# Optimization experiments

Measured on AMD Instinct MI355X. Metric: run time of the kernel, lower is better.

The kernel has to match this reference:

```python
import jax, jax.numpy as jnp
import numpy as np

N_NODES = 50000
N_EDGES = 800000
IN_DIM = 256
HID = 256
NUM_LAYERS = 2


def _sage(xin, src, dst, inv_deg, W_l, b_l, W_r):
    # PyG SAGEConv (mean aggr): lin_l(mean of src features scattered to dst) + lin_r(x)
    agg = jax.ops.segment_sum(xin[src], dst, num_segments=xin.shape[0]) * inv_deg
    return agg @ W_l + b_l + xin @ W_r


def _mgdsgu(x, src, dst, inv_deg, h, Wx_l, bx_l, Wx_r, Wh_l, bh_l, Wh_r, Wb1, bb1, Wb2, bb2):
    # hid->hid conv order: 0=sage_hidden, 1=sage_single_h, 2=sage_update_h, 3=sage_candidate_h
    # in ->hid conv order: 0=sage_single_x, 1=sage_update_x, 2=sage_candidate_x
    h_N = _sage(h, src, dst, inv_deg, Wh_l[0], bh_l[0], Wh_r[0])
    # predict_missing_info: r = zeros so r_v = beta; gamma is computed in the
    # original but multiplied by zero -> no effect (omitted).
    beta = jnp.tanh(h @ Wb1 + bb1 + h_N @ Wb2 + bb2)
    m = h + beta - h_N
    h_N = h_N + m  # == h + beta, kept as written for clarity
    r = jax.nn.sigmoid(_sage(x, src, dst, inv_deg, Wx_l[0], bx_l[0], Wx_r[0])
                       + _sage(h_N, src, dst, inv_deg, Wh_l[1], bh_l[1], Wh_r[1]))
    z = jax.nn.sigmoid(_sage(x, src, dst, inv_deg, Wx_l[1], bx_l[1], Wx_r[1])
                       + _sage(h_N, src, dst, inv_deg, Wh_l[2], bh_l[2], Wh_r[2]))
    h_tilde = jnp.tanh(_sage(x, src, dst, inv_deg, Wx_l[2], bx_l[2], Wx_r[2])
                       + _sage(r * h_N, src, dst, inv_deg, Wh_l[3], bh_l[3], Wh_r[3]))
    return (1.0 - z) * h_N + z * h_tilde


def setup_inputs() -> dict:
    key = jax.random.key(0)
    ks = jax.random.split(key, 12)
    sx = 1.0 / np.sqrt(IN_DIM)
    sh = 1.0 / np.sqrt(HID)
    inp = {
        "x": jax.random.normal(ks[0], (N_NODES, IN_DIM), dtype=jnp.float32),
        "edge_index": jax.random.randint(ks[1], (2, N_EDGES), 0, N_NODES, dtype=jnp.int64),
        "Wx_l": jax.random.normal(ks[2], (3, IN_DIM, HID), dtype=jnp.float32) * sx,
        "bx_l": jnp.zeros((3, HID), dtype=jnp.float32),
        "Wx_r": jax.random.normal(ks[3], (3, IN_DIM, HID), dtype=jnp.float32) * sx,
        "Wh_l": jax.random.normal(ks[4], (4, HID, HID), dtype=jnp.float32) * sh,
        "bh_l": jnp.zeros((4, HID), dtype=jnp.float32),
        "Wh_r": jax.random.normal(ks[5], (4, HID, HID), dtype=jnp.float32) * sh,
        "Wb1": jax.random.normal(ks[6], (HID, HID), dtype=jnp.float32) * sh,
        "bb1": jnp.zeros((HID,), dtype=jnp.float32),
        "Wb2": jax.random.normal(ks[7], (HID, HID), dtype=jnp.float32) * sh,
        "bb2": jnp.zeros((HID,), dtype=jnp.float32),
        "We1": jax.random.normal(ks[8], (2 * HID, HID), dtype=jnp.float32) * (1.0 / np.sqrt(2 * HID)),
        "be1": jnp.zeros((HID,), dtype=jnp.float32),
        "We2": jax.random.normal(ks[9], (HID, 1), dtype=jnp.float32) * sh,
        "be2": jnp.zeros((1,), dtype=jnp.float32),
    }
    return inp


def reference(x, edge_index, Wx_l, bx_l, Wx_r, Wh_l, bh_l, Wh_r,
              Wb1, bb1, Wb2, bb2, We1, be1, We2, be2):
    src, dst = edge_index[0], edge_index[1]
    deg = jax.ops.segment_sum(jnp.ones((src.shape[0],), dtype=x.dtype), dst,
                              num_segments=x.shape[0])
    inv_deg = (1.0 / jnp.maximum(deg, 1.0))[:, None]  # [N, 1]

    h = jnp.zeros((x.shape[0], HID), dtype=x.dtype)
    for _ in range(NUM_LAYERS):
        h = _mgdsgu(x, src, dst, inv_deg, h, Wx_l, bx_l, Wx_r,
                    Wh_l, bh_l, Wh_r, Wb1, bb1, Wb2, bb2)

    # edge embeddings: concat(src emb, dst emb) -> MLP -> sigmoid
    edge_emb = jnp.concatenate([h[src], h[dst]], axis=1)  # [E, 2H]
    hidden = jax.nn.relu(edge_emb @ We1 + be1)
    preds = jax.nn.sigmoid(hidden @ We2 + be2)  # [E, 1]
    return (preds, h)
```

## Files before the change

### kernel.cpp

```cpp
#include <hip/hip_runtime.h>
#include <math.h>

#define HID 256

typedef __bf16 bf16x8 __attribute__((ext_vector_type(8)));
typedef float  f32x4  __attribute__((ext_vector_type(4)));

__device__ __forceinline__ float sigmoidf_(float x){ return 1.0f/(1.0f + __expf(-x)); }
__device__ __forceinline__ unsigned short f2b(float f){
  __bf16 b = (__bf16)f; return __builtin_bit_cast(unsigned short, b);
}
__device__ __forceinline__ float b2f(unsigned short u){
  return (float)__builtin_bit_cast(__bf16, u);
}

__device__ __forceinline__ int edge_src(const int* ei, int e, int is64){
  return is64 ? ei[2*e] : ei[e];
}
__device__ __forceinline__ int edge_dst(const int* ei, int e, int E, int is64){
  return is64 ? ei[2*(E+e)] : ei[E+e];
}

__global__ void detect_kernel(const int* __restrict__ ei, int* __restrict__ flag){
  __shared__ int any;
  if (threadIdx.x == 0) any = 0;
  __syncthreads();
  if (ei[2*threadIdx.x + 1] != 0) atomicOr(&any, 1);
  __syncthreads();
  if (threadIdx.x == 0) *flag = any ? 0 : 1;
}

__global__ void count_kernel(const int* __restrict__ ei, const int* __restrict__ flag,
                             int* __restrict__ deg_i, int E){
  int e = blockIdx.x*blockDim.x + threadIdx.x;
  if (e >= E) return;
  int is64 = *flag;
  atomicAdd(&deg_i[edge_dst(ei,e,E,is64)], 1);
}

__global__ __launch_bounds__(1024) void scan_kernel(const int* __restrict__ deg_i,
  int* __restrict__ row_ptr, float* __restrict__ inv_deg, int N)
{
  __shared__ int wsum[16];
  __shared__ int carry_s;
  int tid = threadIdx.x, lane = tid & 63, wid = tid >> 6;
  if (tid == 0) carry_s = 0;
  __syncthreads();
  for (int base = 0; base < N; base += 1024){
    int i = base + tid;
    int v = (i < N) ? deg_i[i] : 0;
    int s = v;
    #pragma unroll
    for (int off = 1; off < 64; off <<= 1){
      int t = __shfl_up(s, off, 64);
      if (lane >= off) s += t;
    }
    if (lane == 63) wsum[wid] = s;
    __syncthreads();
    if (tid == 0){
      int run = 0;
      for (int w2 = 0; w2 < 16; ++w2){ int t = wsum[w2]; wsum[w2] = run; run += t; }
    }
    __syncthreads();
    int excl = carry_s + wsum[wid] + s - v;
    if (i < N){
      row_ptr[i] = excl;
      inv_deg[i] = 1.0f / fmaxf((float)v, 1.0f);
    }
    __syncthreads();
    if (tid == 1023) carry_s = excl + v;
    __syncthreads();
  }
  if (threadIdx.x == 0) row_ptr[N] = carry_s;
}

__global__ void fill_kernel(const int* __restrict__ ei, const int* __restrict__ flag,
                            const int* __restrict__ row_ptr, int* __restrict__ cursor,
                            int* __restrict__ col_src, int E){
  int e = blockIdx.x*blockDim.x + threadIdx.x;
  if (e >= E) return;
  int is64 = *flag;
  int d = edge_dst(ei,e,E,is64);
  int pos = atomicAdd(&cursor[d], 1);
  col_src[row_ptr[d] + pos] = edge_src(ei,e,is64);
}

__global__ __launch_bounds__(256) void conv_kernel(const float* __restrict__ in,
                                                   unsigned short* __restrict__ out, int n4){
  int i = blockIdx.x*256 + threadIdx.x;
  if (i >= n4) return;
  float4 v = *(const float4*)&in[(size_t)i*4];
  ushort4 o; o.x=f2b(v.x); o.y=f2b(v.y); o.z=f2b(v.z); o.w=f2b(v.w);
  *(ushort4*)&out[(size_t)i*4] = o;
}

__global__ __launch_bounds__(256) void wconv_kernel(
  const float* __restrict__ Wx_l, const float* __restrict__ Wx_r,
  const float* __restrict__ Wh_l, const float* __restrict__ Wh_r,
  const float* __restrict__ Wb1,  const float* __restrict__ Wb2,
  const float* __restrict__ We1,  unsigned short* __restrict__ Wt)
{
  int widx = blockIdx.x;
  int n = blockIdx.y;
  int k = threadIdx.x;
  const float* src;
  if      (widx < 3)  src = Wx_l + widx*65536;
  else if (widx < 6)  src = Wx_r + (widx-3)*65536;
  else if (widx < 10) src = Wh_l + (widx-6)*65536;
  else if (widx < 14) src = Wh_r + (widx-10)*65536;
  else if (widx == 14) src = Wb1;
  else if (widx == 15) src = Wb2;
  else                src = We1 + (widx-16)*65536;
  Wt[(size_t)widx*65536 + n*256 + k] = f2b(src[k*256 + n]);
}

__global__ __launch_bounds__(256) void aggregate_b_kernel(
    const unsigned short* __restrict__ X, unsigned short* __restrict__ out,
    const int* __restrict__ row_ptr, const int* __restrict__ col_src,
    const float* __restrict__ inv_deg, int N)
{
  int v = blockIdx.x*4 + (threadIdx.x >> 6);
  int lane = threadIdx.x & 63;
  if (v >= N) return;
  int beg = row_ptr[v], end = row_ptr[v+1];
  float a0=0.f, a1=0.f, a2=0.f, a3=0.f;
  int e = beg;
  for (; e + 4 <= end; e += 4){
    int s0 = col_src[e], s1 = col_src[e+1], s2 = col_src[e+2], s3 = col_src[e+3];
    ushort4 u0 = *(const ushort4*)&X[(size_t)s0*HID + lane*4];
    ushort4 u1 = *(const ushort4*)&X[(size_t)s1*HID + lane*4];
    ushort4 u2 = *(const ushort4*)&X[(size_t)s2*HID + lane*4];
    ushort4 u3 = *(const ushort4*)&X[(size_t)s3*HID + lane*4];
    a0 += b2f(u0.x)+b2f(u1.x)+b2f(u2.x)+b2f(u3.x);
    a1 += b2f(u0.y)+b2f(u1.y)+b2f(u2.y)+b2f(u3.y);
    a2 += b2f(u0.z)+b2f(u1.z)+b2f(u2.z)+b2f(u3.z);
    a3 += b2f(u0.w)+b2f(u1.w)+b2f(u2.w)+b2f(u3.w);
  }
  for (; e < end; ++e){
    int s0 = col_src[e];
    ushort4 u0 = *(const ushort4*)&X[(size_t)s0*HID + lane*4];
    a0 += b2f(u0.x); a1 += b2f(u0.y); a2 += b2f(u0.z); a3 += b2f(u0.w);
  }
  float w = inv_deg[v];
  ushort4 o; o.x=f2b(a0*w); o.y=f2b(a1*w); o.z=f2b(a2*w); o.w=f2b(a3*w);
  *(ushort4*)&out[(size_t)v*HID + lane*4] = o;
}

__global__ __launch_bounds__(256) void rowprep_kernel(
  const float* __restrict__ bh_l, const float* __restrict__ bb1, const float* __restrict__ bb2,
  const float* __restrict__ Wb2, const float* __restrict__ Wh_l, const float* __restrict__ Wh_r,
  float* __restrict__ hrow, float* __restrict__ rowL1, float* __restrict__ rowR1,
  float* __restrict__ rowL2, float* __restrict__ rowR2)
{
  __shared__ float sh[256];
  __shared__ float sh2[256];
  int j = threadIdx.x;
  sh[j] = bh_l[j];
  __syncthreads();
  float acc = bb1[j] + bb2[j];
  for (int k = 0; k < 256; ++k) acc = fmaf(sh[k], Wb2[k*256 + j], acc);
  float hr = tanhf(acc);
  hrow[j] = hr; sh2[j] = hr;
  __syncthreads();
  const float* Whl1 = Wh_l + 65536;  const float* Whr1 = Wh_r + 65536;
  const float* Whl2 = Wh_l + 131072; const float* Whr2 = Wh_r + 131072;
  float a1=0.f, b1=0.f, a2=0.f, b2v=0.f;
  for (int k = 0; k < 256; ++k){
    float hv = sh2[k];
    a1  = fmaf(hv, Whl1[k*256+j], a1);
    b1  = fmaf(hv, Whr1[k*256+j], b1);
    a2  = fmaf(hv, Whl2[k*256+j], a2);
    b2v = fmaf(hv, Whr2[k*256+j], b2v);
  }
  rowL1[j] = a1; rowR1[j] = b1 + bh_l[256 + j];
  rowL2[j] = a2; rowR2[j] = b2v + bh_l[512 + j];
}

template<int MODE>
__global__ __launch_bounds__(256) void mgemm_kernel(
    const unsigned short* __restrict__ A0, const unsigned short* __restrict__ W0,
    const unsigned short* __restrict__ A1, const unsigned short* __restrict__ W1,
    const unsigned short* __restrict__ A2, const unsigned short* __restrict__ W2,
    const unsigned short* __restrict__ A3, const unsigned short* __restrict__ W3,
    const float* __restrict__ bias, const float* __restrict__ bias2,
    const float* Z, const float* HN, int hn_bcast,
    const float* __restrict__ rowA, const float* __restrict__ rowB,
    const float* __restrict__ mulrow, const float* mulmat,
    const int* __restrict__ deg,
    float* outF, unsigned short* outB, int M)
{
  __shared__ unsigned short Al[128*32];
  __shared__ unsigned short Bl[128*32];
  const int tid  = threadIdx.x;
  const int lane = tid & 63, w = tid >> 6;
  const int wr = w >> 1, wc = w & 1;
  const int lane15 = lane & 15, laneq = (lane >> 4) * 8;
  const int row0 = blockIdx.x * 128, col0 = blockIdx.y * 128;

  f32x4 acc[4][4];
  #pragma unroll
  for (int m = 0; m < 4; ++m)
    #pragma unroll
    for (int n = 0; n < 4; ++n) acc[m][n] = (f32x4)0.f;

  const unsigned short* pa[4]; const unsigned short* pw[4];
  int np = 0;
  if (A0){ pa[np]=A0; pw[np]=W0; ++np; }
  if (A1){ pa[np]=A1; pw[np]=W1; ++np; }
  if (A2){ pa[np]=A2; pw[np]=W2; ++np; }
  if (A3){ pa[np]=A3; pw[np]=W3; ++np; }
  const int steps = np * 8;

  const int srow = tid >> 1;
  const int koff = (tid & 1) * 16;
  const int arow = (row0 + srow > M-1) ? (M-1) : (row0 + srow);

  uint4 ra0, ra1, rb0, rb1;
  {
    const unsigned short* Ap = pa[0];
    const unsigned short* Wp = pw[0];
    const unsigned short* ga = Ap + (size_t)arow*HID + koff;
    const unsigned short* gb = Wp + (size_t)(col0 + srow)*HID + koff;
    ra0 = *(const uint4*)(ga);  ra1 = *(const uint4*)(ga + 8);
    rb0 = *(const uint4*)(gb);  rb1 = *(const uint4*)(gb + 8);
  }

  for (int s = 0; s < steps; ++s){
    __syncthreads();
    *(uint4*)&Al[tid*16]     = ra0;
    *(uint4*)&Al[tid*16 + 8] = ra1;
    *(uint4*)&Bl[tid*16]     = rb0;
    *(uint4*)&Bl[tid*16 + 8] = rb1;
    if (s + 1 < steps){
      int sp = s + 1;
      const unsigned short* Ap = pa[sp >> 3];
      const unsigned short* Wp = pw[sp >> 3];
      int k0 = (sp & 7) * 32;
      const unsigned short* ga = Ap + (size_t)arow*HID + k0 + koff;
      const unsigned short* gb = Wp + (size_t)(col0 + srow)*HID + k0 + koff;
      ra0 = *(const uint4*)(ga);  ra1 = *(const uint4*)(ga + 8);
      rb0 = *(const uint4*)(gb);  rb1 = *(const uint4*)(gb + 8);
    }
    __syncthreads();

    bf16x8 af[4], bfr[4];
    #pragma unroll
    for (int m = 0; m < 4; ++m)
      af[m] = *(const bf16x8*)&Al[(wr*64 + m*16 + lane15)*32 + laneq];
    #pragma unroll
    for (int n = 0; n < 4; ++n)
      bfr[n] = *(const bf16x8*)&Bl[(wc*64 + n*16 + lane15)*32 + laneq];
    #pragma unroll
    for (int m = 0; m < 4; ++m)
      #pragma unroll
      for (int n = 0; n < 4; ++n)
        acc[m][n] = __builtin_amdgcn_mfma_f32_16x16x32_bf16(af[m], bfr[n], acc[m][n], 0, 0, 0);
  }

  #pragma unroll
  for (int n = 0; n < 4; ++n){
    int gc = col0 + wc*64 + n*16 + lane15;
    float badd = 0.f;
    if (bias)  badd += bias[gc];
    if (bias2) badd += bias2[gc];
    float rA = 0.f, rB = 0.f, mr = 1.f, hnb = 0.f;
    if (MODE == 1){
      if (rowA){ rA = rowA[gc]; rB = rowB[gc]; }
      if (mulrow) mr = mulrow[gc];
    }
    if (MODE == 3 && hn_bcast) hnb = HN[gc];
    #pragma unroll
    for (int m = 0; m < 4; ++m){
      int rb = row0 + wr*64 + m*16 + ((lane >> 4) << 2);
      #pragma unroll
      for (int r = 0; r < 4; ++r){
        int gr = rb + r;
        if (gr >= M) continue;
        size_t idx = (size_t)gr*HID + gc;
        float p = acc[m][n][r] + badd;
        float v;
        if (MODE == 0) v = p;
        else if (MODE == 1){
          float g = (rowA && deg) ? ((deg[gr] > 0) ? 1.f : 0.f) : 0.f;
          v = sigmoidf_(p + g*rA + rB);
          if (mulrow) v *= mr;
          if (mulmat) v *= mulmat[idx];
        } else if (MODE == 2){
          v = HN[idx] + tanhf(p);
        } else {
          float z  = Z[idx];
          float hv = hn_bcast ? hnb : HN[idx];
          v = (1.f - z)*hv + z*tanhf(p);
        }
        if (outF) outF[idx] = v;
        if (outB) outB[idx] = f2b(v);
      }
    }
  }
}

__global__ __launch_bounds__(256) void edge_pred_kernel(
  const unsigned short* __restrict__ P, const unsigned short* __restrict__ Q,
  const int* __restrict__ ei, const int* __restrict__ flag,
  const float* __restrict__ We2, const float* __restrict__ be2,
  float* __restrict__ preds, int E)
{
  int wid = blockIdx.x*4 + (threadIdx.x >> 6);
  int lane = threadIdx.x & 63;
  if (wid >= E) return;
  int is64 = *flag;
  int s = edge_src(ei, wid, is64);
  int d = edge_dst(ei, wid, E, is64);
  ushort4 p4 = *(const ushort4*)&P[(size_t)s*HID + lane*4];
  ushort4 q4 = *(const ushort4*)&Q[(size_t)d*HID + lane*4];
  float4 w = *(const float4*)&We2[lane*4];
  float h0 = fmaxf(b2f(p4.x) + b2f(q4.x), 0.f);
  float h1 = fmaxf(b2f(p4.y) + b2f(q4.y), 0.f);
  float h2 = fmaxf(b2f(p4.z) + b2f(q4.z), 0.f);
  float h3 = fmaxf(b2f(p4.w) + b2f(q4.w), 0.f);
  float part = h0*w.x + h1*w.y + h2*w.z + h3*w.w;
  #pragma unroll
  for (int off = 32; off > 0; off >>= 1) part += __shfl_down(part, off, 64);
  if (lane == 0) preds[wid] = sigmoidf_(part + be2[0]);
}

typedef const unsigned short* cus;
typedef const float* cf;

static void launch_mg(int mode,
  cus A0, cus W0, cus A1, cus W1, cus A2, cus W2, cus A3, cus W3,
  cf bias, cf bias2, cf Z, cf HN, int hn_bcast,
  cf rowA, cf rowB, cf mulrow, cf mulmat, const int* deg,
  float* outF, unsigned short* outB, int M, hipStream_t s)
{
  dim3 g((M + 127)/128, 2), b(256);
  switch (mode){
    case 0: mgemm_kernel<0><<<g,b,0,s>>>(A0,W0,A1,W1,A2,W2,A3,W3,bias,bias2,Z,HN,hn_bcast,rowA,rowB,mulrow,mulmat,deg,outF,outB,M); break;
    case 1: mgemm_kernel<1><<<g,b,0,s>>>(A0,W0,A1,W1,A2,W2,A3,W3,bias,bias2,Z,HN,hn_bcast,rowA,rowB,mulrow,mulmat,deg,outF,outB,M); break;
    case 2: mgemm_kernel<2><<<g,b,0,s>>>(A0,W0,A1,W1,A2,W2,A3,W3,bias,bias2,Z,HN,hn_bcast,rowA,rowB,mulrow,mulmat,deg,outF,outB,M); break;
    default:mgemm_kernel<3><<<g,b,0,s>>>(A0,W0,A1,W1,A2,W2,A3,W3,bias,bias2,Z,HN,hn_bcast,rowA,rowB,mulrow,mulmat,deg,outF,outB,M); break;
  }
}

extern "C" void kernel_launch(void* const* d_in, const int* in_sizes, int n_in,
                              void* d_out, int out_size, void* d_ws, size_t ws_size,
                              hipStream_t stream)
{
  const float* x    = (const float*)d_in[0];
  const int*   ei   = (const int*)  d_in[1];
  const float* Wx_l = (const float*)d_in[2];
  const float* bx_l = (const float*)d_in[3];
  const float* Wx_r = (const float*)d_in[4];
  const float* Wh_l = (const float*)d_in[5];
  const float* bh_l = (const float*)d_in[6];
  const float* Wh_r = (const float*)d_in[7];
  const float* Wb1  = (const float*)d_in[8];
  const float* bb1  = (const float*)d_in[9];
  const float* Wb2  = (const float*)d_in[10];
  const float* bb2  = (const float*)d_in[11];
  const float* We1  = (const float*)d_in[12];
  const float* be1  = (const float*)d_in[13];
  const float* We2  = (const float*)d_in[14];
  const float* be2  = (const float*)d_in[15];

  const int N = in_sizes[0] / HID;
  const int E = in_sizes[1] / 2;
  cf NUL = nullptr; cus NUB = nullptr; const int* NULI = nullptr;

  size_t off = 0;
  auto alloc = [&](size_t bytes) -> void* {
    void* p = (char*)d_ws + off;
    off += (bytes + 255) & ~(size_t)255;
    return p;
  };
  int*   deg_i   = (int*)  alloc((size_t)N*4);
  int*   cursor  = (int*)  alloc((size_t)N*4);
  int*   row_ptr = (int*)  alloc(((size_t)N+1)*4);
  int*   col_src = (int*)  alloc((size_t)E*4);
  float* inv_deg = (float*)alloc((size_t)N*4);
  int*   flag    = (int*)  alloc(256);
  float* hrow    = (float*)alloc(1024);
  float* rowL1   = (float*)alloc(1024);
  float* rowR1   = (float*)alloc(1024);
  float* rowL2   = (float*)alloc(1024);
  float* rowR2   = (float*)alloc(1024);
  unsigned short* Wt = (unsigned short*)alloc((size_t)18*65536*2);
  float* F0 = (float*)alloc((size_t)N*HID*4);
  float* F1 = (float*)alloc((size_t)N*HID*4);
  unsigned short* b0 = (unsigned short*)alloc((size_t)N*HID*2);
  unsigned short* b1 = (unsigned short*)alloc((size_t)N*HID*2);
  unsigned short* b2 = (unsigned short*)alloc((size_t)N*HID*2);
  unsigned short* b3 = (unsigned short*)alloc((size_t)N*HID*2);
  unsigned short* b4 = (unsigned short*)alloc((size_t)N*HID*2);

  float* preds = (float*)d_out;
  float* H     = preds + E;

  auto WT = [&](int i) -> cus { return Wt + (size_t)i*65536; };
  const float* bx0 = bx_l;  const float* bx1 = bx_l + 256; const float* bx2 = bx_l + 512;
  const float* bh0 = bh_l;  const float* bh1 = bh_l + 256;
  const float* bh2 = bh_l + 512; const float* bh3 = bh_l + 768;

  const int eb  = (E + 255)/256;
  const int nb4 = (N + 3)/4;
  const int n4b = (N*64 + 255)/256;

  hipMemsetAsync(deg_i, 0, (size_t)N*4, stream);
  hipMemsetAsync(cursor, 0, (size_t)N*4, stream);
  detect_kernel<<<1,256,0,stream>>>(ei, flag);
  count_kernel<<<eb,256,0,stream>>>(ei, flag, deg_i, E);
  scan_kernel<<<1,1024,0,stream>>>(deg_i, row_ptr, inv_deg, N);
  fill_kernel<<<eb,256,0,stream>>>(ei, flag, row_ptr, cursor, col_src, E);

  conv_kernel<<<n4b,256,0,stream>>>(x, b0, N*64);
  wconv_kernel<<<dim3(18,256),256,0,stream>>>(Wx_l, Wx_r, Wh_l, Wh_r, Wb1, Wb2, We1, Wt);
  rowprep_kernel<<<1,256,0,stream>>>(bh_l, bb1, bb2, Wb2, Wh_l, Wh_r,
                                     hrow, rowL1, rowR1, rowL2, rowR2);

  aggregate_b_kernel<<<nb4,256,0,stream>>>(b0, b1, row_ptr, col_src, inv_deg, N);
  launch_mg(1, b1,WT(0), b0,WT(3), NUB,NUB, NUB,NUB, bx0,NUL, NUL,NUL,0,
            rowL1,rowR1, hrow,NUL, deg_i, nullptr, b2, N, stream);
  launch_mg(1, b1,WT(1), b0,WT(4), NUB,NUB, NUB,NUB, bx1,NUL, NUL,NUL,0,
            rowL2,rowR2, NUL,NUL, deg_i, F0, nullptr, N, stream);
  aggregate_b_kernel<<<nb4,256,0,stream>>>(b2, b3, row_ptr, col_src, inv_deg, N);
  launch_mg(3, b3,WT(9), b2,WT(13), b1,WT(2), b0,WT(5), bx2,bh3, F0,hrow,1,
            NUL,NUL, NUL,NUL, NULI, F0, b4, N, stream);

  aggregate_b_kernel<<<nb4,256,0,stream>>>(b4, b2, row_ptr, col_src, inv_deg, N);
  launch_mg(0, b2,WT(6), b4,WT(10), NUB,NUB, NUB,NUB, bh0,NUL, NUL,NUL,0,
            NUL,NUL, NUL,NUL, NULI, nullptr, b3, N, stream);
  launch_mg(2, b4,WT(14), b3,WT(15), NUB,NUB, NUB,NUB, bb1,bb2, NUL,F0,0,
            NUL,NUL, NUL,NUL, NULI, F1, b2, N, stream);
  aggregate_b_kernel<<<nb4,256,0,stream>>>(b2, b3, row_ptr, col_src, inv_deg, N);
  launch_mg(1, b3,WT(7), b2,WT(11), b1,WT(0), b0,WT(3), bx0,bh1, NUL,NUL,0,
            NUL,NUL, NUL,F1, NULI, nullptr, b4, N, stream);
  launch_mg(1, b3,WT(8), b2,WT(12), b1,WT(1), b0,WT(4), bx1,bh2, NUL,NUL,0,
            NUL,NUL, NUL,NUL, NULI, F0, nullptr, N, stream);
  aggregate_b_kernel<<<nb4,256,0,stream>>>(b4, b3, row_ptr, col_src, inv_deg, N);
  launch_mg(3, b3,WT(9), b4,WT(13), b1,WT(2), b0,WT(5), bx2,bh3, F0,F1,0,
            NUL,NUL, NUL,NUL, NULI, H, b2, N, stream);

  launch_mg(0, b2,WT(16), NUB,NUB, NUB,NUB, NUB,NUB, be1,NUL, NUL,NUL,0,
            NUL,NUL, NUL,NUL, NULI, nullptr, b3, N, stream);
  launch_mg(0, b2,WT(17), NUB,NUB, NUB,NUB, NUB,NUB, NUL,NUL, NUL,NUL,0,
            NUL,NUL, NUL,NUL, NULI, nullptr, b4, N, stream);
  edge_pred_kernel<<<(E+3)/4,256,0,stream>>>(b3, b4, ei, flag, We2, be2, preds, E);
}
```

Baseline: 1.366 ms.

## Fold hidden SAGE into beta GEMM, widen GEMM K-tile, retune aggregation and edge kernels

Precomposes Wh_l[0]·Wb2 and Wh_r[0]·Wb2+Wb1 into combined weights, so the second layer's h_N GEMM is eliminated and beta is computed directly from the aggregated h and h. The matrix GEMM now stages 64-wide K tiles with an XOR-swizzled shared layout, halving the number of sync steps and aiming to avoid LDS bank conflicts. The aggregation loop unrolls to 8 gathers per iteration, and edge prediction uses 32 lanes per edge with 8-wide loads. Composing weights in bf16 changes rounding slightly, and h_N is no longer materialized, so the data flow between buffers was rewired.

```diff
diff --git a/kernel.cpp b/kernel.cpp
--- a/kernel.cpp
+++ b/kernel.cpp
@@ -5,6 +5,7 @@
 
 typedef __bf16 bf16x8 __attribute__((ext_vector_type(8)));
 typedef float  f32x4  __attribute__((ext_vector_type(4)));
+typedef unsigned short us8 __attribute__((ext_vector_type(8)));
 
 __device__ __forceinline__ float sigmoidf_(float x){ return 1.0f/(1.0f + __expf(-x)); }
 __device__ __forceinline__ unsigned short f2b(float f){
@@ -114,6 +115,20 @@
   Wt[(size_t)widx*65536 + n*256 + k] = f2b(src[k*256 + n]);
 }
 
+__global__ __launch_bounds__(256) void comp_kernel(
+  const float* __restrict__ A, const float* __restrict__ B,
+  const float* __restrict__ add, unsigned short* __restrict__ dst)
+{
+  __shared__ float col[256];
+  int n = blockIdx.x, k = threadIdx.x;
+  col[k] = B[k*256 + n];
+  __syncthreads();
+  float s = add ? add[k*256 + n] : 0.f;
+  #pragma unroll 8
+  for (int j = 0; j < 256; ++j) s = fmaf(A[k*256 + j], col[j], s);
+  dst[n*256 + k] = f2b(s);
+}
+
 __global__ __launch_bounds__(256) void aggregate_b_kernel(
     const unsigned short* __restrict__ X, unsigned short* __restrict__ out,
     const int* __restrict__ row_ptr, const int* __restrict__ col_src,
@@ -125,21 +140,20 @@
   int beg = row_ptr[v], end = row_ptr[v+1];
   float a0=0.f, a1=0.f, a2=0.f, a3=0.f;
   int e = beg;
-  for (; e + 4 <= end; e += 4){
-    int s0 = col_src[e], s1 = col_src[e+1], s2 = col_src[e+2], s3 = col_src[e+3];
-    ushort4 u0 = *(const ushort4*)&X[(size_t)s0*HID + lane*4];
-    ushort4 u1 = *(const ushort4*)&X[(size_t)s1*HID + lane*4];
-    ushort4 u2 = *(const ushort4*)&X[(size_t)s2*HID + lane*4];
-    ushort4 u3 = *(const ushort4*)&X[(size_t)s3*HID + lane*4];
-    a0 += b2f(u0.x)+b2f(u1.x)+b2f(u2.x)+b2f(u3.x);
-    a1 += b2f(u0.y)+b2f(u1.y)+b2f(u2.y)+b2f(u3.y);
-    a2 += b2f(u0.z)+b2f(u1.z)+b2f(u2.z)+b2f(u3.z);
-    a3 += b2f(u0.w)+b2f(u1.w)+b2f(u2.w)+b2f(u3.w);
+  for (; e + 8 <= end; e += 8){
+    int sidx[8];
+    #pragma unroll
+    for (int t = 0; t < 8; ++t) sidx[t] = col_src[e + t];
+    #pragma unroll
+    for (int t = 0; t < 8; ++t){
+      ushort4 u = *(const ushort4*)&X[(size_t)sidx[t]*HID + lane*4];
+      a0 += b2f(u.x); a1 += b2f(u.y); a2 += b2f(u.z); a3 += b2f(u.w);
+    }
   }
   for (; e < end; ++e){
     int s0 = col_src[e];
-    ushort4 u0 = *(const ushort4*)&X[(size_t)s0*HID + lane*4];
-    a0 += b2f(u0.x); a1 += b2f(u0.y); a2 += b2f(u0.z); a3 += b2f(u0.w);
+    ushort4 u = *(const ushort4*)&X[(size_t)s0*HID + lane*4];
+    a0 += b2f(u.x); a1 += b2f(u.y); a2 += b2f(u.z); a3 += b2f(u.w);
   }
   float w = inv_deg[v];
   ushort4 o; o.x=f2b(a0*w); o.y=f2b(a1*w); o.z=f2b(a2*w); o.w=f2b(a3*w);
@@ -149,7 +163,8 @@
 __global__ __launch_bounds__(256) void rowprep_kernel(
   const float* __restrict__ bh_l, const float* __restrict__ bb1, const float* __restrict__ bb2,
   const float* __restrict__ Wb2, const float* __restrict__ Wh_l, const float* __restrict__ Wh_r,
-  float* __restrict__ hrow, float* __restrict__ rowL1, float* __restrict__ rowR1,
+  float* __restrict__ brow, float* __restrict__ hrow,
+  float* __restrict__ rowL1, float* __restrict__ rowR1,
   float* __restrict__ rowL2, float* __restrict__ rowR2)
 {
   __shared__ float sh[256];
@@ -160,6 +175,7 @@
   float acc = bb1[j] + bb2[j];
   for (int k = 0; k < 256; ++k) acc = fmaf(sh[k], Wb2[k*256 + j], acc);
   float hr = tanhf(acc);
+  brow[j] = acc;
   hrow[j] = hr; sh2[j] = hr;
   __syncthreads();
   const float* Whl1 = Wh_l + 65536;  const float* Whr1 = Wh_r + 65536;
@@ -189,12 +205,12 @@
     const int* __restrict__ deg,
     float* outF, unsigned short* outB, int M)
 {
-  __shared__ unsigned short Al[128*32];
-  __shared__ unsigned short Bl[128*32];
+  __shared__ unsigned short Al[128*64];
+  __shared__ unsigned short Bl[128*64];
   const int tid  = threadIdx.x;
   const int lane = tid & 63, w = tid >> 6;
   const int wr = w >> 1, wc = w & 1;
-  const int lane15 = lane & 15, laneq = (lane >> 4) * 8;
+  const int lane15 = lane & 15;
   const int row0 = blockIdx.x * 128, col0 = blockIdx.y * 128;
 
   f32x4 acc[4][4];
@@ -209,52 +225,67 @@
   if (A1){ pa[np]=A1; pw[np]=W1; ++np; }
   if (A2){ pa[np]=A2; pw[np]=W2; ++np; }
   if (A3){ pa[np]=A3; pw[np]=W3; ++np; }
-  const int steps = np * 8;
-
-  const int srow = tid >> 1;
-  const int koff = (tid & 1) * 16;
-  const int arow = (row0 + srow > M-1) ? (M-1) : (row0 + srow);
-
-  uint4 ra0, ra1, rb0, rb1;
+  const int steps = np * 4;
+
+  const int trow  = tid >> 3;
+  const int tcole = (tid & 7) * 8;
+  const int scb   = (tcole*2) ^ ((trow & 7) << 4);
+  size_t baseA[4]; size_t baseB[4];
+  #pragma unroll
+  for (int r = 0; r < 4; ++r){
+    int gr = row0 + r*32 + trow; if (gr > M-1) gr = M-1;
+    baseA[r] = (size_t)gr * HID;
+    baseB[r] = (size_t)(col0 + r*32 + trow) * HID;
+  }
+  const int rswz = (lane & 7) << 4;
+  const int cb0  = ((lane >> 4) << 4);
+
+  uint4 ra[4], rb[4];
   {
     const unsigned short* Ap = pa[0];
     const unsigned short* Wp = pw[0];
-    const unsigned short* ga = Ap + (size_t)arow*HID + koff;
-    const unsigned short* gb = Wp + (size_t)(col0 + srow)*HID + koff;
-    ra0 = *(const uint4*)(ga);  ra1 = *(const uint4*)(ga + 8);
-    rb0 = *(const uint4*)(gb);  rb1 = *(const uint4*)(gb + 8);
+    #pragma unroll
+    for (int r = 0; r < 4; ++r){
+      ra[r] = *(const uint4*)(Ap + baseA[r] + tcole);
+      rb[r] = *(const uint4*)(Wp + baseB[r] + tcole);
+    }
   }
 
   for (int s = 0; s < steps; ++s){
     __syncthreads();
-    *(uint4*)&Al[tid*16]     = ra0;
-    *(uint4*)&Al[tid*16 + 8] = ra1;
-    *(uint4*)&Bl[tid*16]     = rb0;
-    *(uint4*)&Bl[tid*16 + 8] = rb1;
+    #pragma unroll
+    for (int r = 0; r < 4; ++r){
+      *(uint4*)((char*)Al + (r*32 + trow)*128 + scb) = ra[r];
+      *(uint4*)((char*)Bl + (r*32 + trow)*128 + scb) = rb[r];
+    }
     if (s + 1 < steps){
       int sp = s + 1;
-      const unsigned short* Ap = pa[sp >> 3];
-      const unsigned short* Wp = pw[sp >> 3];
-      int k0 = (sp & 7) * 32;
-      const unsigned short* ga = Ap + (size_t)arow*HID + k0 + koff;
-      const unsigned short* gb = Wp + (size_t)(col0 + srow)*HID + k0 + koff;
-      ra0 = *(const uint4*)(ga);  ra1 = *(const uint4*)(ga + 8);
-      rb0 = *(const uint4*)(gb);  rb1 = *(const uint4*)(gb + 8);
-    }
-    __syncthreads();
-
-    bf16x8 af[4], bfr[4];
-    #pragma unroll
-    for (int m = 0; m < 4; ++m)
-      af[m] = *(const bf16x8*)&Al[(wr*64 + m*16 + lane15)*32 + laneq];
-    #pragma unroll
-    for (int n = 0; n < 4; ++n)
-      bfr[n] = *(const bf16x8*)&Bl[(wc*64 + n*16 + lane15)*32 + laneq];
-    #pragma unroll
-    for (int m = 0; m < 4; ++m)
+      const unsigned short* Ap = pa[sp >> 2];
+      const unsigned short* Wp = pw[sp >> 2];
+      int k0 = (sp & 3) * 64;
+      #pragma unroll
+      for (int r = 0; r < 4; ++r){
+        ra[r] = *(const uint4*)(Ap + baseA[r] + k0 + tcole);
+        rb[r] = *(const uint4*)(Wp + baseB[r] + k0 + tcole);
+      }
+    }
+    __syncthreads();
+
+    #pragma unroll
+    for (int ks = 0; ks < 2; ++ks){
+      bf16x8 af[4], bfr[4];
+      #pragma unroll
+      for (int m = 0; m < 4; ++m)
+        af[m] = *(const bf16x8*)((const char*)Al + (wr*64 + m*16 + lane15)*128 + ((ks*64 + cb0) ^ rswz));
       #pragma unroll
       for (int n = 0; n < 4; ++n)
-        acc[m][n] = __builtin_amdgcn_mfma_f32_16x16x32_bf16(af[m], bfr[n], acc[m][n], 0, 0, 0);
+        bfr[n] = *(const bf16x8*)((const char*)Bl + (wc*64 + n*16 + lane15)*128 + ((ks*64 + cb0) ^ rswz));
+      #pragma unroll
+      for (int m = 0; m < 4; ++m)
+        #pragma unroll
+        for (int n = 0; n < 4; ++n)
+          acc[m][n] = __builtin_amdgcn_mfma_f32_16x16x32_bf16(af[m], bfr[n], acc[m][n], 0, 0, 0);
+    }
   }
 
   #pragma unroll
@@ -271,10 +302,10 @@
     if (MODE == 3 && hn_bcast) hnb = HN[gc];
     #pragma unroll
     for (int m = 0; m < 4; ++m){
-      int rb = row0 + wr*64 + m*16 + ((lane >> 4) << 2);
+      int rbase = row0 + wr*64 + m*16 + ((lane >> 4) << 2);
       #pragma unroll
       for (int r = 0; r < 4; ++r){
-        int gr = rb + r;
+        int gr = rbase + r;
         if (gr >= M) continue;
         size_t idx = (size_t)gr*HID + gc;
         float p = acc[m][n][r] + badd;
@@ -305,23 +336,26 @@
   const float* __restrict__ We2, const float* __restrict__ be2,
   float* __restrict__ preds, int E)
 {
-  int wid = blockIdx.x*4 + (threadIdx.x >> 6);
-  int lane = threadIdx.x & 63;
+  int wid = blockIdx.x*8 + (threadIdx.x >> 5);
+  int l = threadIdx.x & 31;
   if (wid >= E) return;
   int is64 = *flag;
   int s = edge_src(ei, wid, is64);
   int d = edge_dst(ei, wid, E, is64);
-  ushort4 p4 = *(const ushort4*)&P[(size_t)s*HID + lane*4];
-  ushort4 q4 = *(const ushort4*)&Q[(size_t)d*HID + lane*4];
-  float4 w = *(const float4*)&We2[lane*4];
-  float h0 = fmaxf(b2f(p4.x) + b2f(q4.x), 0.f);
-  float h1 = fmaxf(b2f(p4.y) + b2f(q4.y), 0.f);
-  float h2 = fmaxf(b2f(p4.z) + b2f(q4.z), 0.f);
-  float h3 = fmaxf(b2f(p4.w) + b2f(q4.w), 0.f);
-  float part = h0*w.x + h1*w.y + h2*w.z + h3*w.w;
-  #pragma unroll
-  for (int off = 32; off > 0; off >>= 1) part += __shfl_down(part, off, 64);
-  if (lane == 0) preds[wid] = sigmoidf_(part + be2[0]);
+  us8 p8 = *(const us8*)&P[(size_t)s*HID + l*8];
+  us8 q8 = *(const us8*)&Q[(size_t)d*HID + l*8];
+  float4 w0 = *(const float4*)&We2[l*8];
+  float4 w1 = *(const float4*)&We2[l*8 + 4];
+  float part = 0.f;
+  #pragma unroll
+  for (int j = 0; j < 4; ++j)
+    part = fmaf(fmaxf(b2f(p8[j]) + b2f(q8[j]), 0.f), (&w0.x)[j], part);
+  #pragma unroll
+  for (int j = 0; j < 4; ++j)
+    part = fmaf(fmaxf(b2f(p8[4+j]) + b2f(q8[4+j]), 0.f), (&w1.x)[j], part);
+  #pragma unroll
+  for (int off = 16; off > 0; off >>= 1) part += __shfl_down(part, off, 32);
+  if (l == 0) preds[wid] = sigmoidf_(part + be2[0]);
 }
 
 typedef const unsigned short* cus;
@@ -379,6 +413,7 @@
   int*   col_src = (int*)  alloc((size_t)E*4);
   float* inv_deg = (float*)alloc((size_t)N*4);
   int*   flag    = (int*)  alloc(256);
+  float* brow    = (float*)alloc(1024);
   float* hrow    = (float*)alloc(1024);
   float* rowL1   = (float*)alloc(1024);
   float* rowR1   = (float*)alloc(1024);
@@ -414,8 +449,10 @@
 
   conv_kernel<<<n4b,256,0,stream>>>(x, b0, N*64);
   wconv_kernel<<<dim3(18,256),256,0,stream>>>(Wx_l, Wx_r, Wh_l, Wh_r, Wb1, Wb2, We1, Wt);
+  comp_kernel<<<256,256,0,stream>>>(Wh_l, Wb2, nullptr, (unsigned short*)WT(14));
+  comp_kernel<<<256,256,0,stream>>>(Wh_r, Wb2, Wb1,     (unsigned short*)WT(15));
   rowprep_kernel<<<1,256,0,stream>>>(bh_l, bb1, bb2, Wb2, Wh_l, Wh_r,
-                                     hrow, rowL1, rowR1, rowL2, rowR2);
+                                     brow, hrow, rowL1, rowR1, rowL2, rowR2);
 
   aggregate_b_kernel<<<nb4,256,0,stream>>>(b0, b1, row_ptr, col_src, inv_deg, N);
   launch_mg(1, b1,WT(0), b0,WT(3), NUB,NUB, NUB,NUB, bx0,NUL, NUL,NUL,0,
@@ -427,22 +464,20 @@
             NUL,NUL, NUL,NUL, NULI, F0, b4, N, stream);
 
   aggregate_b_kernel<<<nb4,256,0,stream>>>(b4, b2, row_ptr, col_src, inv_deg, N);
-  launch_mg(0, b2,WT(6), b4,WT(10), NUB,NUB, NUB,NUB, bh0,NUL, NUL,NUL,0,
-            NUL,NUL, NUL,NUL, NULI, nullptr, b3, N, stream);
-  launch_mg(2, b4,WT(14), b3,WT(15), NUB,NUB, NUB,NUB, bb1,bb2, NUL,F0,0,
-            NUL,NUL, NUL,NUL, NULI, F1, b2, N, stream);
-  aggregate_b_kernel<<<nb4,256,0,stream>>>(b2, b3, row_ptr, col_src, inv_deg, N);
-  launch_mg(1, b3,WT(7), b2,WT(11), b1,WT(0), b0,WT(3), bx0,bh1, NUL,NUL,0,
+  launch_mg(2, b2,WT(14), b4,WT(15), NUB,NUB, NUB,NUB, brow,NUL, NUL,F0,0,
+            NUL,NUL, NUL,NUL, NULI, F1, b3, N, stream);
+  aggregate_b_kernel<<<nb4,256,0,stream>>>(b3, b2, row_ptr, col_src, inv_deg, N);
+  launch_mg(1, b2,WT(7), b3,WT(11), b1,WT(0), b0,WT(3), bx0,bh1, NUL,NUL,0,
             NUL,NUL, NUL,F1, NULI, nullptr, b4, N, stream);
-  launch_mg(1, b3,WT(8), b2,WT(12), b1,WT(1), b0,WT(4), bx1,bh2, NUL,NUL,0,
+  launch_mg(1, b2,WT(8), b3,WT(12), b1,WT(1), b0,WT(4), bx1,bh2, NUL,NUL,0,
             NUL,NUL, NUL,NUL, NULI, F0, nullptr, N, stream);
-  aggregate_b_kernel<<<nb4,256,0,stream>>>(b4, b3, row_ptr, col_src, inv_deg, N);
-  launch_mg(3, b3,WT(9), b4,WT(13), b1,WT(2), b0,WT(5), bx2,bh3, F0,F1,0,
-            NUL,NUL, NUL,NUL, NULI, H, b2, N, stream);
-
-  launch_mg(0, b2,WT(16), NUB,NUB, NUB,NUB, NUB,NUB, be1,NUL, NUL,NUL,0,
-            NUL,NUL, NUL,NUL, NULI, nullptr, b3, N, stream);
-  launch_mg(0, b2,WT(17), NUB,NUB, NUB,NUB, NUB,NUB, NUL,NUL, NUL,NUL,0,
+  aggregate_b_kernel<<<nb4,256,0,stream>>>(b4, b2, row_ptr, col_src, inv_deg, N);
+  launch_mg(3, b2,WT(9), b4,WT(13), b1,WT(2), b0,WT(5), bx2,bh3, F0,F1,0,
+            NUL,NUL, NUL,NUL, NULI, H, b3, N, stream);
+
+  launch_mg(0, b3,WT(16), NUB,NUB, NUB,NUB, NUB,NUB, be1,NUL, NUL,NUL,0,
+            NUL,NUL, NUL,NUL, NULI, nullptr, b2, N, stream);
+  launch_mg(0, b3,WT(17), NUB,NUB, NUB,NUB, NUB,NUB, NUL,NUL, NUL,NUL,0,
             NUL,NUL, NUL,NUL, NULI, nullptr, b4, N, stream);
-  edge_pred_kernel<<<(E+3)/4,256,0,stream>>>(b3, b4, ei, flag, We2, be2, preds, E);
-}
+  edge_pred_kernel<<<(E+7)/8,256,0,stream>>>(b2, b4, ei, flag, We2, be2, preds, E);
+}
```

After: 1.995 ms. 1.46x slower.
